# Optimization experiments

Measured on AMD Instinct MI355X. Metric: run time of the kernel, lower is better.

## Reference

```python
import jax, jax.numpy as jnp
import numpy as np

DIM = 1024
E = 8
HID = 4 * DIM  # DomainExpert FFN hidden size


def setup_inputs() -> dict:
    key = jax.random.key(0)
    ks = jax.random.split(key, 7)
    x = jax.random.normal(ks[0], (1, 2048, DIM), dtype=jnp.float32)
    Wr = jax.random.normal(ks[1], (DIM, E), dtype=jnp.float32) * (DIM ** -0.5)
    br = jnp.zeros((E,), dtype=jnp.float32)
    W1 = jax.random.normal(ks[2], (E, DIM, HID), dtype=jnp.float32) * (DIM ** -0.5)
    b1 = jnp.zeros((E, 1, HID), dtype=jnp.float32)
    W2 = jax.random.normal(ks[3], (E, HID, DIM), dtype=jnp.float32) * (HID ** -0.5)
    b2 = jnp.zeros((E, 1, DIM), dtype=jnp.float32)
    return {"x": x, "Wr": Wr, "br": br, "W1": W1, "b1": b1, "W2": W2, "b2": b2}


def reference(x, Wr, br, W1, b1, W2, b2):
    B, T, D = x.shape
    flat = x.reshape(B * T, D)                       # [N, D]
    logits = flat @ Wr + br                          # [N, E]
    z_loss = jnp.mean(jax.nn.logsumexp(logits, axis=-1) ** 2)
    probs = jax.nn.softmax(logits, axis=-1)          # eval path (no Gumbel)
    top_p, top_i = jax.lax.top_k(probs, 2)           # [N, 2]
    top_p = top_p / (top_p.sum(-1, keepdims=True) + 1e-12)
    N = flat.shape[0]
    nE = Wr.shape[1]
    # combine weights: w[t, e] = renormalized top-2 prob if e selected, else 0
    w = jnp.zeros((N, nE), dtype=flat.dtype).at[
        jnp.arange(N)[:, None], top_i].add(top_p)   # [N, E]
    # dense (jit-friendly) expert compute; combine masks out unselected experts
    h = jax.nn.gelu(jnp.einsum('td,edh->teh', flat, W1) + b1.transpose(1, 0, 2))  # [N, E, HID]
    y = jnp.einsum('teh,ehd->ted', h, W2) + b2.transpose(1, 0, 2)                 # [N, E, D]
    out = jnp.einsum('ted,te->td', y, w).reshape(B, T, D)
    importance = probs.mean(axis=0)                                               # [E]
    fi = jax.nn.one_hot(top_i, nE, dtype=flat.dtype).sum(axis=1).mean(axis=0)     # [E]
    aux_loss = jnp.asarray(nE, flat.dtype) * (importance * fi).sum()
    return out, z_loss, aux_loss
```

## Files before the change

### kernel.cpp

```cpp
#include <hip/hip_runtime.h>
#include <math.h>

#define N_TOK 2048
#define DIM   1024
#define NEXP  8
#define HID   4096
#define TOTPAIR (2 * N_TOK)

#define BM 128
#define BN 128
#define BK 32
#define KSPLIT2 4

typedef __bf16 bf16x8 __attribute__((ext_vector_type(8)));
typedef __bf16 bf16x4 __attribute__((ext_vector_type(4)));
typedef float  f32x4  __attribute__((ext_vector_type(4)));

__device__ __forceinline__ float gelu_tanh(float v) {
    float a = 0.7978845608028654f * (v + 0.044715f * v * v * v);
    a = fminf(fmaxf(a, -15.f), 15.f);
    float t = __expf(-2.f * a);
    return 0.5f * v * (1.f + (1.f - t) / (1.f + t));
}

__device__ __forceinline__ void stage16(const __bf16* g, __bf16* lds_base, int lane) {
#if defined(__has_builtin) && __has_builtin(__builtin_amdgcn_global_load_lds)
    __builtin_amdgcn_global_load_lds((const __attribute__((address_space(1))) void*)g,
                                     (__attribute__((address_space(3))) void*)lds_base,
                                     16, 0, 0);
#else
    *(bf16x8*)((char*)lds_base + (size_t)lane * 16) = *(const bf16x8*)g;
#endif
}

__device__ __forceinline__ int expert_prefix(const int* cnt, int e) {
    int s = 0;
    for (int i = 0; i < NEXP; i++) s += (i < e) ? cnt[i] : 0;
    return s;
}

__device__ __forceinline__ void router_body(
    int t, int lane,
    const float* __restrict__ x, const float* __restrict__ Wr, const float* __restrict__ br,
    float* __restrict__ probs, float* __restrict__ lsq,
    int* __restrict__ cnt, int* __restrict__ tok, float* __restrict__ wl) {
    const float* xr = x + (size_t)t * DIM;
    float acc[NEXP];
#pragma unroll
    for (int e = 0; e < NEXP; e++) acc[e] = 0.f;
    for (int d = lane; d < DIM; d += 64) {
        float xv = xr[d];
        const float* wr = Wr + (size_t)d * NEXP;
#pragma unroll
        for (int e = 0; e < NEXP; e++) acc[e] = fmaf(xv, wr[e], acc[e]);
    }
#pragma unroll
    for (int off = 32; off >= 1; off >>= 1) {
#pragma unroll
        for (int e = 0; e < NEXP; e++) acc[e] += __shfl_xor(acc[e], off, 64);
    }
    if (lane == 0) {
        float lg[NEXP], mx = -1e30f;
#pragma unroll
        for (int e = 0; e < NEXP; e++) { lg[e] = acc[e] + br[e]; mx = fmaxf(mx, lg[e]); }
        float se = 0.f, p[NEXP];
#pragma unroll
        for (int e = 0; e < NEXP; e++) { p[e] = expf(lg[e] - mx); se += p[e]; }
        float inv = 1.f / se;
        float lse = mx + logf(se);
        lsq[t] = lse * lse;
#pragma unroll
        for (int e = 0; e < NEXP; e++) probs[t * NEXP + e] = p[e] * inv;
        int i0 = 0;
#pragma unroll
        for (int e = 1; e < NEXP; e++) if (p[e] > p[i0]) i0 = e;
        int i1 = (i0 == 0) ? 1 : 0;
#pragma unroll
        for (int e = 0; e < NEXP; e++) if (e != i0 && p[e] > p[i1]) i1 = e;
        float p0 = p[i0] * inv, p1 = p[i1] * inv;
        float rn = 1.f / (p0 + p1 + 1e-12f);
        int pos0 = atomicAdd(&cnt[i0], 1);
        tok[i0 * N_TOK + pos0] = t;
        wl[i0 * N_TOK + pos0] = p0 * rn;
        int pos1 = atomicAdd(&cnt[i1], 1);
        tok[i1 * N_TOK + pos1] = t;
        wl[i1 * N_TOK + pos1] = p1 * rn;
    }
}

__global__ void router_kernel(const float* __restrict__ x, const float* __restrict__ Wr,
                              const float* __restrict__ br,
                              float* __restrict__ probs, float* __restrict__ lsq,
                              int* __restrict__ cnt, int* __restrict__ tok,
                              float* __restrict__ wl) {
    router_body(blockIdx.x, threadIdx.x, x, Wr, br, probs, lsq, cnt, tok, wl);
}

#define PREP_ROUTER 512
#define PREP_CONV   2048
#define PREP_T1     8192
#define PREP_T2     8192

__global__ __launch_bounds__(256) void prep_kernel(
    const float* __restrict__ x, const float* __restrict__ Wr, const float* __restrict__ br,
    float* __restrict__ probs, float* __restrict__ lsq,
    int* __restrict__ cnt, int* __restrict__ tok, float* __restrict__ wl,
    __bf16* __restrict__ xb,
    const float* __restrict__ W1, __bf16* __restrict__ W1T,
    const float* __restrict__ W2, __bf16* __restrict__ W2T) {
    __shared__ __bf16 tile[64][68];
    const int b = blockIdx.x;
    const int tid = threadIdx.x;

    if (b < PREP_ROUTER) {
        int t = b * 4 + (tid >> 6);
        router_body(t, tid & 63, x, Wr, br, probs, lsq, cnt, tok, wl);
        return;
    }
    if (b < PREP_ROUTER + PREP_CONV) {
        int idx = (b - PREP_ROUTER) * 256 + tid;
        float4 v = ((const float4*)x)[idx];
        bf16x4 o;
        o.x = (__bf16)v.x; o.y = (__bf16)v.y; o.z = (__bf16)v.z; o.w = (__bf16)v.w;
        ((bf16x4*)xb)[idx] = o;
        return;
    }
    const float* in; __bf16* out; int R, C, bx, by, bz;
    if (b < PREP_ROUTER + PREP_CONV + PREP_T1) {
        int bb = b - (PREP_ROUTER + PREP_CONV);
        in = W1; out = W1T; R = DIM; C = HID;
        bx = bb & 63; by = (bb >> 6) & 15; bz = bb >> 10;
    } else {
        int bb = b - (PREP_ROUTER + PREP_CONV + PREP_T1);
        in = W2; out = W2T; R = HID; C = DIM;
        bx = bb & 15; by = (bb >> 4) & 63; bz = bb >> 10;
    }
    const size_t eoff = (size_t)bz * (size_t)R * (size_t)C;
    const int rb = by * 64, cb = bx * 64;
    const int r = tid >> 4, c4 = (tid & 15) * 4;
#pragma unroll
    for (int i = 0; i < 4; i++) {
        int row = r + i * 16;
        float4 v = *(const float4*)(in + eoff + (size_t)(rb + row) * C + cb + c4);
        bf16x4 o;
        o.x = (__bf16)v.x; o.y = (__bf16)v.y; o.z = (__bf16)v.z; o.w = (__bf16)v.w;
        *(bf16x4*)&tile[row][c4] = o;
    }
    __syncthreads();
    const int c = tid >> 2, ch0 = tid & 3;
#pragma unroll
    for (int i = 0; i < 2; i++) {
        int ch = ch0 + i * 4;
        bf16x8 o;
#pragma unroll
        for (int j = 0; j < 8; j++) o[j] = tile[ch * 8 + j][c];
        *(bf16x8*)(out + eoff + (size_t)(cb + c) * R + rb + ch * 8) = o;
    }
}

__global__ __launch_bounds__(256, 4) void gemm1_kernel(
    const __bf16* __restrict__ xb, const __bf16* __restrict__ W1T,
    const float* __restrict__ b1,
    const int* __restrict__ cnt,
    const int* __restrict__ tok, __bf16* __restrict__ h) {
    const int L = blockIdx.x;
    const int xcd = L & 7;
    const int r1 = L >> 3;
    const int n = r1 & 31;
    const int key = (r1 >> 5) * 8 + xcd;
    const int e = key >> 4;
    const int m = key & 15;
    const int ce = cnt[e];
    const int mstart = m * BM;
    if (mstart >= ce) return;
    const int n0 = n * BN;
    const int offe = expert_prefix(cnt, e);

    __shared__ __bf16 smem[BM * 128];
    __shared__ int toksh[BM];
    __bf16* As = smem;
    __bf16* Bs = smem + BM * BK;

    const int tid = threadIdx.x;
    if (tid < BM) {
        int idx = mstart + tid;
        toksh[tid] = (idx < ce) ? tok[e * N_TOK + idx] : 0;
    }
    __syncthreads();

    const int lane = tid & 63;
    const int wid  = tid >> 6;
    const int row0 = (wid >> 1) * 64;
    const int col0 = (wid & 1) * 64;
    const int quad = lane >> 4;
    const int lcol = lane & 15;

    const int sub = lane >> 2;
    const int gk  = (((lane & 3) ^ (sub & 3)) << 3);
    const int ra0 = wid * 32 + sub;
    const int ra1 = ra0 + 16;

    const __bf16* __restrict__ W1e = W1T + (size_t)e * HID * DIM;
    const __bf16* pA0 = xb + (size_t)toksh[ra0] * DIM + gk;
    const __bf16* pA1 = xb + (size_t)toksh[ra1] * DIM + gk;
    const __bf16* pB0 = W1e + (size_t)(n0 + ra0) * DIM + gk;
    const __bf16* pB1 = W1e + (size_t)(n0 + ra1) * DIM + gk;
    __bf16* lA0 = &As[(wid * 2 + 0) * 512];
    __bf16* lA1 = &As[(wid * 2 + 1) * 512];
    __bf16* lB0 = &Bs[(wid * 2 + 0) * 512];
    __bf16* lB1 = &Bs[(wid * 2 + 1) * 512];

    const int swz = (quad ^ (lcol & 3)) << 3;
    const __bf16* aF = &As[(row0 + lcol) * BK + swz];
    const __bf16* bF = &Bs[(col0 + lcol) * BK + swz];

    f32x4 acc[4][4];
#pragma unroll
    for (int i = 0; i < 4; i++)
#pragma unroll
        for (int j = 0; j < 4; j++) acc[i][j] = (f32x4){0.f, 0.f, 0.f, 0.f};

    for (int k0 = 0; k0 < DIM; k0 += BK) {
        stage16(pA0 + k0, lA0, lane);
        stage16(pA1 + k0, lA1, lane);
        stage16(pB0 + k0, lB0, lane);
        stage16(pB1 + k0, lB1, lane);
        __syncthreads();
        bf16x8 af[4], bfr[4];
#pragma unroll
        for (int i = 0; i < 4; i++) af[i]  = *(const bf16x8*)(aF + i * 16 * BK);
#pragma unroll
        for (int j = 0; j < 4; j++) bfr[j] = *(const bf16x8*)(bF + j * 16 * BK);
#pragma unroll
        for (int i = 0; i < 4; i++)
#pragma unroll
            for (int j = 0; j < 4; j++)
                acc[i][j] = __builtin_amdgcn_mfma_f32_16x16x32_bf16(af[i], bfr[j], acc[i][j], 0, 0, 0);
        __syncthreads();
    }

    const float* __restrict__ b1e = b1 + (size_t)e * HID;
    float bj[4];
#pragma unroll
    for (int j = 0; j < 4; j++) bj[j] = b1e[n0 + col0 + j * 16 + lcol];
#pragma unroll
    for (int i = 0; i < 4; i++)
#pragma unroll
        for (int reg = 0; reg < 4; reg++) {
            int row = row0 + i * 16 + quad * 4 + reg;
#pragma unroll
            for (int j = 0; j < 4; j++) {
                int col = col0 + j * 16 + lcol;
                int slot = (col >> 3) ^ (row & 15);
                smem[row * 128 + slot * 8 + (col & 7)] =
                    (__bf16)gelu_tanh(acc[i][j][reg] + bj[j]);
            }
        }
    __syncthreads();
    {
        int row = tid >> 1, half = tid & 1;
        int pos = mstart + row;
        if (pos < ce) {
            __bf16* hp = h + (size_t)(offe + pos) * HID + n0 + half * 64;
#pragma unroll
            for (int j = 0; j < 8; j++) {
                int chunk = half * 8 + j;
                int slot = chunk ^ (row & 15);
                *(bf16x8*)(hp + j * 8) = *(const bf16x8*)&smem[row * 128 + slot * 8];
            }
        }
    }
}

__global__ __launch_bounds__(256, 4) void gemm2_kernel(
    const __bf16* __restrict__ h, const __bf16* __restrict__ W2T,
    const float* __restrict__ b2,
    const int* __restrict__ cnt,
    const int* __restrict__ tok, const float* __restrict__ wl,
    float* __restrict__ out) {
    const int L = blockIdx.x;
    const int xcd = L & 7;
    const int r1 = L >> 3;
    const int inner = r1 & 31;
    const int key = (r1 >> 5) * 8 + xcd;
    const int e = key >> 4;
    const int m = key & 15;
    const int n = inner & 7;
    const int split = inner >> 3;
    const int ce = cnt[e];
    const int mstart = m * BM;
    if (mstart >= ce) return;
    const int n0 = n * BN;
    const int ks = split * (HID / KSPLIT2);
    const int offe = expert_prefix(cnt, e);

    __shared__ __bf16 As[BM * BK];
    __shared__ __bf16 Bs[BN * BK];
    __shared__ int   toksh[BM];
    __shared__ float wsh[BM];

    const int tid = threadIdx.x;
    if (tid < BM) {
        int idx = mstart + tid;
        toksh[tid] = (idx < ce) ? tok[e * N_TOK + idx] : 0;
        wsh[tid]   = (idx < ce) ? wl[e * N_TOK + idx] : 0.f;
    }
    __syncthreads();

    const int lane = tid & 63;
    const int wid  = tid >> 6;
    const int row0 = (wid >> 1) * 64;
    const int col0 = (wid & 1) * 64;
    const int quad = lane >> 4;
    const int lcol = lane & 15;

    const int sub = lane >> 2;
    const int gk  = (((lane & 3) ^ (sub & 3)) << 3);
    const int ra0 = wid * 32 + sub;
    const int ra1 = ra0 + 16;

    int hr0 = offe + mstart + ra0; if (hr0 >= TOTPAIR) hr0 = TOTPAIR - 1;
    int hr1 = offe + mstart + ra1; if (hr1 >= TOTPAIR) hr1 = TOTPAIR - 1;

    const __bf16* __restrict__ W2e = W2T + (size_t)e * DIM * HID;
    const __bf16* pA0 = h + (size_t)hr0 * HID + ks + gk;
    const __bf16* pA1 = h + (size_t)hr1 * HID + ks + gk;
    const __bf16* pB0 = W2e + (size_t)(n0 + ra0) * HID + ks + gk;
    const __bf16* pB1 = W2e + (size_t)(n0 + ra1) * HID + ks + gk;
    __bf16* lA0 = &As[(wid * 2 + 0) * 512];
    __bf16* lA1 = &As[(wid * 2 + 1) * 512];
    __bf16* lB0 = &Bs[(wid * 2 + 0) * 512];
    __bf16* lB1 = &Bs[(wid * 2 + 1) * 512];

    const int swz = (quad ^ (lcol & 3)) << 3;
    const __bf16* aF = &As[(row0 + lcol) * BK + swz];
    const __bf16* bF = &Bs[(col0 + lcol) * BK + swz];

    f32x4 acc[4][4];
#pragma unroll
    for (int i = 0; i < 4; i++)
#pragma unroll
        for (int j = 0; j < 4; j++) acc[i][j] = (f32x4){0.f, 0.f, 0.f, 0.f};

    for (int k0 = 0; k0 < HID / KSPLIT2; k0 += BK) {
        stage16(pA0 + k0, lA0, lane);
        stage16(pA1 + k0, lA1, lane);
        stage16(pB0 + k0, lB0, lane);
        stage16(pB1 + k0, lB1, lane);
        __syncthreads();
        bf16x8 af[4], bfr[4];
#pragma unroll
        for (int i = 0; i < 4; i++) af[i]  = *(const bf16x8*)(aF + i * 16 * BK);
#pragma unroll
        for (int j = 0; j < 4; j++) bfr[j] = *(const bf16x8*)(bF + j * 16 * BK);
#pragma unroll
        for (int i = 0; i < 4; i++)
#pragma unroll
            for (int j = 0; j < 4; j++)
                acc[i][j] = __builtin_amdgcn_mfma_f32_16x16x32_bf16(af[i], bfr[j], acc[i][j], 0, 0, 0);
        __syncthreads();
    }

    const float* __restrict__ b2e = b2 + (size_t)e * DIM;
    const bool addBias = (split == 0);
#pragma unroll
    for (int i = 0; i < 4; i++) {
#pragma unroll
        for (int reg = 0; reg < 4; reg++) {
            int lrow = row0 + i * 16 + quad * 4 + reg;
            int pos = mstart + lrow;
            if (pos >= ce) continue;
            int tokm = toksh[lrow];
            float w = wsh[lrow];
#pragma unroll
            for (int j = 0; j < 4; j++) {
                int gcol = n0 + col0 + j * 16 + lcol;
                float v = acc[i][j][reg] + (addBias ? b2e[gcol] : 0.f);
                atomicAdd(&out[(size_t)tokm * DIM + gcol], w * v);
            }
        }
    }
}

__global__ __launch_bounds__(256, 2) void ffn_fallback_kernel(
    const float* __restrict__ x,
    const float* __restrict__ W1, const float* __restrict__ b1,
    const float* __restrict__ W2, const float* __restrict__ b2,
    const int* __restrict__ cnt, const int* __restrict__ tok,
    const float* __restrict__ wl, float* __restrict__ out) {
    const int e = blockIdx.y;
    const int ce = cnt[e];
    const int start = blockIdx.x * 16;
    if (start >= ce) return;
    __shared__ float hs[16][128];
    __shared__ int toks[16];
    __shared__ float wgt[16];
    const int tid = threadIdx.x;
    if (tid < 16) {
        int idx = start + tid;
        if (idx < ce) { toks[tid] = tok[e * N_TOK + idx]; wgt[tid] = wl[e * N_TOK + idx]; }
        else          { toks[tid] = -1;                   wgt[tid] = 0.f; }
    }
    __syncthreads();
    const float* __restrict__ W1e = W1 + (size_t)e * DIM * HID;
    const float* __restrict__ W2e = W2 + (size_t)e * HID * DIM;
    const int am  = tid >> 4;
    const int aj0 = (tid & 15) * 8;
    const int at  = toks[am];
    const float* __restrict__ xrow = x + (size_t)(at < 0 ? 0 : at) * DIM;
    const int n0 = tid * 4;
    float acc[16][4];
#pragma unroll
    for (int m = 0; m < 16; m++)
#pragma unroll
        for (int i = 0; i < 4; i++) acc[m][i] = 0.f;
    for (int c = 0; c < HID; c += 128) {
        float ha[8];
#pragma unroll
        for (int r = 0; r < 8; r++) ha[r] = 0.f;
        const float* wp = W1e + c + aj0;
        for (int d = 0; d < DIM; d += 4) {
            float4 xv = *(const float4*)(xrow + d);
#pragma unroll
            for (int k = 0; k < 4; k++) {
                const float* wr = wp + (size_t)(d + k) * HID;
                float4 wa = *(const float4*)(wr);
                float4 wb = *(const float4*)(wr + 4);
                float xk = (k == 0) ? xv.x : (k == 1) ? xv.y : (k == 2) ? xv.z : xv.w;
                ha[0] = fmaf(xk, wa.x, ha[0]); ha[1] = fmaf(xk, wa.y, ha[1]);
                ha[2] = fmaf(xk, wa.z, ha[2]); ha[3] = fmaf(xk, wa.w, ha[3]);
                ha[4] = fmaf(xk, wb.x, ha[4]); ha[5] = fmaf(xk, wb.y, ha[5]);
                ha[6] = fmaf(xk, wb.z, ha[6]); ha[7] = fmaf(xk, wb.w, ha[7]);
            }
        }
        __syncthreads();
#pragma unroll
        for (int r = 0; r < 8; r++) {
            float v = ha[r] + b1[e * HID + c + aj0 + r];
            hs[am][aj0 + r] = gelu_tanh(v);
        }
        __syncthreads();
        for (int jj = 0; jj < 128; jj++) {
            float4 wv = *(const float4*)(W2e + (size_t)(c + jj) * DIM + n0);
#pragma unroll
            for (int m = 0; m < 16; m++) {
                float hv = hs[m][jj];
                acc[m][0] = fmaf(hv, wv.x, acc[m][0]); acc[m][1] = fmaf(hv, wv.y, acc[m][1]);
                acc[m][2] = fmaf(hv, wv.z, acc[m][2]); acc[m][3] = fmaf(hv, wv.w, acc[m][3]);
            }
        }
    }
    const float* bp = b2 + e * DIM + n0;
    float b0 = bp[0], b1v = bp[1], b2v = bp[2], b3 = bp[3];
#pragma unroll 1
    for (int m = 0; m < 16; m++) {
        int t = toks[m];
        if (t < 0) continue;
        float w = wgt[m];
        float* op = out + (size_t)t * DIM + n0;
        atomicAdd(op + 0, w * (acc[m][0] + b0));
        atomicAdd(op + 1, w * (acc[m][1] + b1v));
        atomicAdd(op + 2, w * (acc[m][2] + b2v));
        atomicAdd(op + 3, w * (acc[m][3] + b3));
    }
}

__global__ void finalize_kernel(const float* __restrict__ probs, const float* __restrict__ lsq,
                                const int* __restrict__ cnt, float* __restrict__ scal) {
    __shared__ float part[256][9];
    const int tid = threadIdx.x;
    float z = 0.f;
    float im[NEXP];
#pragma unroll
    for (int e = 0; e < NEXP; e++) im[e] = 0.f;
    for (int t = tid; t < N_TOK; t += 256) {
        z += lsq[t];
#pragma unroll
        for (int e = 0; e < NEXP; e++) im[e] += probs[t * NEXP + e];
    }
    part[tid][0] = z;
#pragma unroll
    for (int e = 0; e < NEXP; e++) part[tid][1 + e] = im[e];
    __syncthreads();
    if (tid == 0) {
        float zs = 0.f, ims[NEXP];
        for (int e = 0; e < NEXP; e++) ims[e] = 0.f;
        for (int i = 0; i < 256; i++) {
            zs += part[i][0];
            for (int e = 0; e < NEXP; e++) ims[e] += part[i][1 + e];
        }
        float nInv = 1.0f / (float)N_TOK;
        float aux = 0.f;
        for (int e = 0; e < NEXP; e++) aux += (ims[e] * nInv) * ((float)cnt[e] * nInv);
        scal[0] = zs * nInv;
        scal[1] = (float)NEXP * aux;
    }
}

extern "C" void kernel_launch(void* const* d_in, const int* in_sizes, int n_in,
                              void* d_out, int out_size, void* d_ws, size_t ws_size,
                              hipStream_t stream) {
    const float* x  = (const float*)d_in[0];
    const float* Wr = (const float*)d_in[1];
    const float* br = (const float*)d_in[2];
    const float* W1 = (const float*)d_in[3];
    const float* b1 = (const float*)d_in[4];
    const float* W2 = (const float*)d_in[5];
    const float* b2 = (const float*)d_in[6];
    float* out = (float*)d_out;

    char* base = (char*)d_ws;
    int*   cnt   = (int*)(base);
    int*   tokp  = (int*)(base + 64);
    float* wlp   = (float*)(base + 64 + 65536);
    float* probs = (float*)(base + 64 + 2 * 65536);
    float* lsq   = (float*)(base + 64 + 3 * 65536);
    const size_t SMALL_END = 64 + 3 * 65536 + 8192;
    __bf16* xb   = (__bf16*)(base + SMALL_END);
    __bf16* W1T  = (__bf16*)(base + SMALL_END + 4194304ull);
    __bf16* W2T  = (__bf16*)(base + SMALL_END + 4194304ull + 67108864ull);
    __bf16* hbuf = (__bf16*)(base + SMALL_END + 4194304ull + 2ull * 67108864ull);
    const size_t REQ = SMALL_END + 4194304ull + 2ull * 67108864ull + 33554432ull;

    hipMemsetAsync(base, 0, 64, stream);
    hipMemsetAsync(d_out, 0, (size_t)out_size * sizeof(float), stream);

    if (ws_size >= REQ) {
        prep_kernel<<<PREP_ROUTER + PREP_CONV + PREP_T1 + PREP_T2, 256, 0, stream>>>(
            x, Wr, br, probs, lsq, cnt, tokp, wlp, xb, W1, W1T, W2, W2T);
        gemm1_kernel<<<4096, 256, 0, stream>>>(xb, W1T, b1, cnt, tokp, hbuf);
        gemm2_kernel<<<4096, 256, 0, stream>>>(hbuf, W2T, b2, cnt, tokp, wlp, out);
    } else {
        router_kernel<<<N_TOK, 64, 0, stream>>>(x, Wr, br, probs, lsq, cnt, tokp, wlp);
        ffn_fallback_kernel<<<dim3(128, NEXP), 256, 0, stream>>>(
            x, W1, b1, W2, b2, cnt, tokp, wlp, out);
    }

    finalize_kernel<<<1, 256, 0, stream>>>(probs, lsq, cnt, out + (size_t)N_TOK * DIM);
}
```

Baseline: 633.8 us.

## Convert fp32 expert weights to bf16 inside GEMM loops instead of prepass transpose

Drops the prepass that transposed W1 and W2 into bf16 copies in the workspace. Each GEMM now reads the fp32 weights in their original row-major layout, converts them to bf16 in registers and writes them into a swizzled shared-memory layout the MFMA fragments can read. This removes a full read-and-write pass over both weight tensors and shrinks the workspace. In exchange each weight tile is read as fp32 (twice the bytes) once per M-tile, and the XCD-aware block-index remapping is replaced by a plain 3D grid.

```diff
diff --git a/kernel.cpp b/kernel.cpp
--- a/kernel.cpp
+++ b/kernel.cpp
@@ -96,90 +96,41 @@
     router_body(blockIdx.x, threadIdx.x, x, Wr, br, probs, lsq, cnt, tok, wl);
 }
 
-#define PREP_ROUTER 512
-#define PREP_CONV   2048
-#define PREP_T1     8192
-#define PREP_T2     8192
-
 __global__ __launch_bounds__(256) void prep_kernel(
     const float* __restrict__ x, const float* __restrict__ Wr, const float* __restrict__ br,
     float* __restrict__ probs, float* __restrict__ lsq,
     int* __restrict__ cnt, int* __restrict__ tok, float* __restrict__ wl,
-    __bf16* __restrict__ xb,
-    const float* __restrict__ W1, __bf16* __restrict__ W1T,
-    const float* __restrict__ W2, __bf16* __restrict__ W2T) {
-    __shared__ __bf16 tile[64][68];
+    __bf16* __restrict__ xb) {
     const int b = blockIdx.x;
     const int tid = threadIdx.x;
-
-    if (b < PREP_ROUTER) {
+    if (b < 512) {
         int t = b * 4 + (tid >> 6);
         router_body(t, tid & 63, x, Wr, br, probs, lsq, cnt, tok, wl);
         return;
     }
-    if (b < PREP_ROUTER + PREP_CONV) {
-        int idx = (b - PREP_ROUTER) * 256 + tid;
-        float4 v = ((const float4*)x)[idx];
-        bf16x4 o;
-        o.x = (__bf16)v.x; o.y = (__bf16)v.y; o.z = (__bf16)v.z; o.w = (__bf16)v.w;
-        ((bf16x4*)xb)[idx] = o;
-        return;
-    }
-    const float* in; __bf16* out; int R, C, bx, by, bz;
-    if (b < PREP_ROUTER + PREP_CONV + PREP_T1) {
-        int bb = b - (PREP_ROUTER + PREP_CONV);
-        in = W1; out = W1T; R = DIM; C = HID;
-        bx = bb & 63; by = (bb >> 6) & 15; bz = bb >> 10;
-    } else {
-        int bb = b - (PREP_ROUTER + PREP_CONV + PREP_T1);
-        in = W2; out = W2T; R = HID; C = DIM;
-        bx = bb & 15; by = (bb >> 4) & 63; bz = bb >> 10;
-    }
-    const size_t eoff = (size_t)bz * (size_t)R * (size_t)C;
-    const int rb = by * 64, cb = bx * 64;
-    const int r = tid >> 4, c4 = (tid & 15) * 4;
-#pragma unroll
-    for (int i = 0; i < 4; i++) {
-        int row = r + i * 16;
-        float4 v = *(const float4*)(in + eoff + (size_t)(rb + row) * C + cb + c4);
-        bf16x4 o;
-        o.x = (__bf16)v.x; o.y = (__bf16)v.y; o.z = (__bf16)v.z; o.w = (__bf16)v.w;
-        *(bf16x4*)&tile[row][c4] = o;
-    }
-    __syncthreads();
-    const int c = tid >> 2, ch0 = tid & 3;
-#pragma unroll
-    for (int i = 0; i < 2; i++) {
-        int ch = ch0 + i * 4;
-        bf16x8 o;
-#pragma unroll
-        for (int j = 0; j < 8; j++) o[j] = tile[ch * 8 + j][c];
-        *(bf16x8*)(out + eoff + (size_t)(cb + c) * R + rb + ch * 8) = o;
-    }
+    int idx = (b - 512) * 256 + tid;
+    float4 v = ((const float4*)x)[idx];
+    bf16x4 o;
+    o.x = (__bf16)v.x; o.y = (__bf16)v.y; o.z = (__bf16)v.z; o.w = (__bf16)v.w;
+    ((bf16x4*)xb)[idx] = o;
 }
 
 __global__ __launch_bounds__(256, 4) void gemm1_kernel(
-    const __bf16* __restrict__ xb, const __bf16* __restrict__ W1T,
+    const __bf16* __restrict__ xb, const float* __restrict__ W1,
     const float* __restrict__ b1,
     const int* __restrict__ cnt,
     const int* __restrict__ tok, __bf16* __restrict__ h) {
-    const int L = blockIdx.x;
-    const int xcd = L & 7;
-    const int r1 = L >> 3;
-    const int n = r1 & 31;
-    const int key = (r1 >> 5) * 8 + xcd;
-    const int e = key >> 4;
-    const int m = key & 15;
+    const int e = blockIdx.z;
     const int ce = cnt[e];
-    const int mstart = m * BM;
+    const int mstart = blockIdx.y * BM;
     if (mstart >= ce) return;
-    const int n0 = n * BN;
+    const int n0 = blockIdx.x * BN;
     const int offe = expert_prefix(cnt, e);
 
     __shared__ __bf16 smem[BM * 128];
     __shared__ int toksh[BM];
     __bf16* As = smem;
-    __bf16* Bs = smem + BM * BK;
+    __bf16* Bs = smem + 4096;
 
     const int tid = threadIdx.x;
     if (tid < BM) {
@@ -199,20 +150,18 @@
     const int gk  = (((lane & 3) ^ (sub & 3)) << 3);
     const int ra0 = wid * 32 + sub;
     const int ra1 = ra0 + 16;
-
-    const __bf16* __restrict__ W1e = W1T + (size_t)e * HID * DIM;
     const __bf16* pA0 = xb + (size_t)toksh[ra0] * DIM + gk;
     const __bf16* pA1 = xb + (size_t)toksh[ra1] * DIM + gk;
-    const __bf16* pB0 = W1e + (size_t)(n0 + ra0) * DIM + gk;
-    const __bf16* pB1 = W1e + (size_t)(n0 + ra1) * DIM + gk;
     __bf16* lA0 = &As[(wid * 2 + 0) * 512];
     __bf16* lA1 = &As[(wid * 2 + 1) * 512];
-    __bf16* lB0 = &Bs[(wid * 2 + 0) * 512];
-    __bf16* lB1 = &Bs[(wid * 2 + 1) * 512];
-
-    const int swz = (quad ^ (lcol & 3)) << 3;
-    const __bf16* aF = &As[(row0 + lcol) * BK + swz];
-    const __bf16* bF = &Bs[(col0 + lcol) * BK + swz];
+
+    const int khalf = (wid >> 1) * 16;
+    const int nl    = (wid & 1) * 64 + lane;
+    const float* __restrict__ W1e = W1 + (size_t)e * DIM * HID;
+    const float* wsrc = W1e + (size_t)khalf * HID + n0 + nl;
+
+    const int aswz = (quad ^ (lcol & 3)) << 3;
+    const __bf16* aF = &As[(row0 + lcol) * BK + aswz];
 
     f32x4 acc[4][4];
 #pragma unroll
@@ -221,16 +170,28 @@
         for (int j = 0; j < 4; j++) acc[i][j] = (f32x4){0.f, 0.f, 0.f, 0.f};
 
     for (int k0 = 0; k0 < DIM; k0 += BK) {
+        float v[16];
+        const float* ws = wsrc + (size_t)k0 * HID;
+#pragma unroll
+        for (int j = 0; j < 16; j++) v[j] = ws[(size_t)j * HID];
         stage16(pA0 + k0, lA0, lane);
         stage16(pA1 + k0, lA1, lane);
-        stage16(pB0 + k0, lB0, lane);
-        stage16(pB1 + k0, lB1, lane);
+#pragma unroll
+        for (int q = 0; q < 4; q++) {
+            bf16x4 pk;
+            pk.x = (__bf16)v[q * 4 + 0]; pk.y = (__bf16)v[q * 4 + 1];
+            pk.z = (__bf16)v[q * 4 + 2]; pk.w = (__bf16)v[q * 4 + 3];
+            int c = (wid >> 1) * 2 + (q >> 1);
+            int slot = c ^ (nl & 3);
+            *(bf16x4*)&Bs[slot * 1024 + nl * 8 + (q & 1) * 4] = pk;
+        }
         __syncthreads();
         bf16x8 af[4], bfr[4];
 #pragma unroll
         for (int i = 0; i < 4; i++) af[i]  = *(const bf16x8*)(aF + i * 16 * BK);
 #pragma unroll
-        for (int j = 0; j < 4; j++) bfr[j] = *(const bf16x8*)(bF + j * 16 * BK);
+        for (int j = 0; j < 4; j++)
+            bfr[j] = *(const bf16x8*)&Bs[((quad ^ (lcol & 3)) * 1024) + (col0 + j * 16 + lcol) * 8];
 #pragma unroll
         for (int i = 0; i < 4; i++)
 #pragma unroll
@@ -273,29 +234,22 @@
 }
 
 __global__ __launch_bounds__(256, 4) void gemm2_kernel(
-    const __bf16* __restrict__ h, const __bf16* __restrict__ W2T,
+    const __bf16* __restrict__ h, const float* __restrict__ W2,
     const float* __restrict__ b2,
     const int* __restrict__ cnt,
     const int* __restrict__ tok, const float* __restrict__ wl,
     float* __restrict__ out) {
-    const int L = blockIdx.x;
-    const int xcd = L & 7;
-    const int r1 = L >> 3;
-    const int inner = r1 & 31;
-    const int key = (r1 >> 5) * 8 + xcd;
-    const int e = key >> 4;
-    const int m = key & 15;
-    const int n = inner & 7;
-    const int split = inner >> 3;
+    const int e = blockIdx.z >> 2;
+    const int split = blockIdx.z & 3;
     const int ce = cnt[e];
-    const int mstart = m * BM;
+    const int mstart = blockIdx.y * BM;
     if (mstart >= ce) return;
-    const int n0 = n * BN;
+    const int n0 = blockIdx.x * BN;
     const int ks = split * (HID / KSPLIT2);
     const int offe = expert_prefix(cnt, e);
 
     __shared__ __bf16 As[BM * BK];
-    __shared__ __bf16 Bs[BN * BK];
+    __shared__ __bf16 Bs[4 * 128 * 8];
     __shared__ int   toksh[BM];
     __shared__ float wsh[BM];
 
@@ -318,23 +272,20 @@
     const int gk  = (((lane & 3) ^ (sub & 3)) << 3);
     const int ra0 = wid * 32 + sub;
     const int ra1 = ra0 + 16;
-
     int hr0 = offe + mstart + ra0; if (hr0 >= TOTPAIR) hr0 = TOTPAIR - 1;
     int hr1 = offe + mstart + ra1; if (hr1 >= TOTPAIR) hr1 = TOTPAIR - 1;
-
-    const __bf16* __restrict__ W2e = W2T + (size_t)e * DIM * HID;
     const __bf16* pA0 = h + (size_t)hr0 * HID + ks + gk;
     const __bf16* pA1 = h + (size_t)hr1 * HID + ks + gk;
-    const __bf16* pB0 = W2e + (size_t)(n0 + ra0) * HID + ks + gk;
-    const __bf16* pB1 = W2e + (size_t)(n0 + ra1) * HID + ks + gk;
     __bf16* lA0 = &As[(wid * 2 + 0) * 512];
     __bf16* lA1 = &As[(wid * 2 + 1) * 512];
-    __bf16* lB0 = &Bs[(wid * 2 + 0) * 512];
-    __bf16* lB1 = &Bs[(wid * 2 + 1) * 512];
-
-    const int swz = (quad ^ (lcol & 3)) << 3;
-    const __bf16* aF = &As[(row0 + lcol) * BK + swz];
-    const __bf16* bF = &Bs[(col0 + lcol) * BK + swz];
+
+    const int khalf = (wid >> 1) * 16;
+    const int nl    = (wid & 1) * 64 + lane;
+    const float* __restrict__ W2e = W2 + (size_t)e * HID * DIM;
+    const float* wsrc = W2e + (size_t)(ks + khalf) * DIM + n0 + nl;
+
+    const int aswz = (quad ^ (lcol & 3)) << 3;
+    const __bf16* aF = &As[(row0 + lcol) * BK + aswz];
 
     f32x4 acc[4][4];
 #pragma unroll
@@ -343,16 +294,28 @@
         for (int j = 0; j < 4; j++) acc[i][j] = (f32x4){0.f, 0.f, 0.f, 0.f};
 
     for (int k0 = 0; k0 < HID / KSPLIT2; k0 += BK) {
+        float v[16];
+        const float* ws = wsrc + (size_t)k0 * DIM;
+#pragma unroll
+        for (int j = 0; j < 16; j++) v[j] = ws[(size_t)j * DIM];
         stage16(pA0 + k0, lA0, lane);
         stage16(pA1 + k0, lA1, lane);
-        stage16(pB0 + k0, lB0, lane);
-        stage16(pB1 + k0, lB1, lane);
+#pragma unroll
+        for (int q = 0; q < 4; q++) {
+            bf16x4 pk;
+            pk.x = (__bf16)v[q * 4 + 0]; pk.y = (__bf16)v[q * 4 + 1];
+            pk.z = (__bf16)v[q * 4 + 2]; pk.w = (__bf16)v[q * 4 + 3];
+            int c = (wid >> 1) * 2 + (q >> 1);
+            int slot = c ^ (nl & 3);
+            *(bf16x4*)&Bs[slot * 1024 + nl * 8 + (q & 1) * 4] = pk;
+        }
         __syncthreads();
         bf16x8 af[4], bfr[4];
 #pragma unroll
         for (int i = 0; i < 4; i++) af[i]  = *(const bf16x8*)(aF + i * 16 * BK);
 #pragma unroll
-        for (int j = 0; j < 4; j++) bfr[j] = *(const bf16x8*)(bF + j * 16 * BK);
+        for (int j = 0; j < 4; j++)
+            bfr[j] = *(const bf16x8*)&Bs[((quad ^ (lcol & 3)) * 1024) + (col0 + j * 16 + lcol) * 8];
 #pragma unroll
         for (int i = 0; i < 4; i++)
 #pragma unroll
@@ -375,8 +338,8 @@
 #pragma unroll
             for (int j = 0; j < 4; j++) {
                 int gcol = n0 + col0 + j * 16 + lcol;
-                float v = acc[i][j][reg] + (addBias ? b2e[gcol] : 0.f);
-                atomicAdd(&out[(size_t)tokm * DIM + gcol], w * v);
+                float vv = acc[i][j][reg] + (addBias ? b2e[gcol] : 0.f);
+                atomicAdd(&out[(size_t)tokm * DIM + gcol], w * vv);
             }
         }
     }
@@ -517,19 +480,19 @@
     float* lsq   = (float*)(base + 64 + 3 * 65536);
     const size_t SMALL_END = 64 + 3 * 65536 + 8192;
     __bf16* xb   = (__bf16*)(base + SMALL_END);
-    __bf16* W1T  = (__bf16*)(base + SMALL_END + 4194304ull);
-    __bf16* W2T  = (__bf16*)(base + SMALL_END + 4194304ull + 67108864ull);
-    __bf16* hbuf = (__bf16*)(base + SMALL_END + 4194304ull + 2ull * 67108864ull);
-    const size_t REQ = SMALL_END + 4194304ull + 2ull * 67108864ull + 33554432ull;
+    __bf16* hbuf = (__bf16*)(base + SMALL_END + 4194304ull);
+    const size_t REQ = SMALL_END + 4194304ull + 33554432ull;
 
     hipMemsetAsync(base, 0, 64, stream);
     hipMemsetAsync(d_out, 0, (size_t)out_size * sizeof(float), stream);
 
     if (ws_size >= REQ) {
-        prep_kernel<<<PREP_ROUTER + PREP_CONV + PREP_T1 + PREP_T2, 256, 0, stream>>>(
-            x, Wr, br, probs, lsq, cnt, tokp, wlp, xb, W1, W1T, W2, W2T);
-        gemm1_kernel<<<4096, 256, 0, stream>>>(xb, W1T, b1, cnt, tokp, hbuf);
-        gemm2_kernel<<<4096, 256, 0, stream>>>(hbuf, W2T, b2, cnt, tokp, wlp, out);
+        prep_kernel<<<512 + 2048, 256, 0, stream>>>(
+            x, Wr, br, probs, lsq, cnt, tokp, wlp, xb);
+        gemm1_kernel<<<dim3(HID / BN, N_TOK / BM, NEXP), 256, 0, stream>>>(
+            xb, W1, b1, cnt, tokp, hbuf);
+        gemm2_kernel<<<dim3(DIM / BN, N_TOK / BM, NEXP * KSPLIT2), 256, 0, stream>>>(
+            hbuf, W2, b2, cnt, tokp, wlp, out);
     } else {
         router_kernel<<<N_TOK, 64, 0, stream>>>(x, Wr, br, probs, lsq, cnt, tokp, wlp);
         ffn_fallback_kernel<<<dim3(128, NEXP), 256, 0, stream>>>(
```

Result: faster. 540.1 us (-14.8%).
